# Performance work log

Hardware: AMD Instinct MI355X
Metric: run time of the kernel (lower is better)

## Reference

```python
import jax, jax.numpy as jnp
import numpy as np

N = 100000        # nodes
E = 1600000       # edges
NFEAT = 512
NLABEL = 64
NHID = 256
L_LAB = 5000


def _lin_init(key, fan_in, fan_out):
    kw, kb = jax.random.split(key)
    s = 1.0 / np.sqrt(fan_in).astype(np.float32)
    W = jax.random.uniform(kw, (fan_in, fan_out), jnp.float32, -s, s)
    b = jax.random.uniform(kb, (fan_out,), jnp.float32, -s, s)
    return W, b


def setup_inputs() -> dict:
    key = jax.random.key(0)
    ks = jax.random.split(key, 10)
    x = jax.random.normal(ks[0], (N, NFEAT), jnp.float32)
    y = jax.random.randint(ks[1], (N,), 0, NLABEL, jnp.int32)
    predictions = jax.random.uniform(ks[2], (N, NLABEL), dtype=jnp.float32)
    adj = jax.random.randint(ks[3], (2, E), 0, N, jnp.int32)
    idx_labeled = jax.random.randint(ks[4], (L_LAB,), 0, N, jnp.int32)
    d_in = NFEAT + NLABEL
    W0, b0 = _lin_init(ks[5], d_in, NHID)
    W1, b1 = _lin_init(ks[6], NHID, NHID)
    W2, b2 = _lin_init(ks[7], NHID, NHID)
    Wm0, bm0 = _lin_init(ks[8], NHID, 2 * NHID)
    Wm1, bm1 = _lin_init(ks[9], 2 * NHID, NLABEL)
    return dict(x=x, y=y, predictions=predictions, adj=adj, idx_labeled=idx_labeled,
                n_sample=1, W0=W0, b0=b0, W1=W1, b1=b1, W2=W2, b2=b2,
                Wm0=Wm0, bm0=bm0, Wm1=Wm1, bm1=bm1)


def reference(x, y, predictions, adj, idx_labeled, n_sample,
              W0, b0, W1, b1, W2, b2, Wm0, bm0, Wm1, bm1):
    n = x.shape[0]
    # --- pre_train label features: one_hot of (nlabel+2)-filled indices, labeled
    # nodes set to y; slicing to :nlabel makes out-of-range rows all-zero, which
    # jax.nn.one_hot does directly. -> [N, NLABEL]
    idx = jnp.full((n,), NLABEL + 2, jnp.int32).at[idx_labeled].set(y[idx_labeled])
    feats = jax.nn.one_hot(idx, NLABEL, dtype=x.dtype)
    h = jnp.concatenate([x, feats], axis=1)  # [N, nfeat+nlabel]

    # --- GCN normalization (improved=True: self-loop weight 2.0)
    loops = jnp.arange(n, dtype=adj.dtype)
    row = jnp.concatenate([adj[0], loops])  # message sources
    col = jnp.concatenate([adj[1], loops])  # aggregation targets
    ew = jnp.concatenate([jnp.ones((adj.shape[1],), jnp.float32),
                          jnp.full((n,), 2.0, jnp.float32)])
    deg = jax.ops.segment_sum(ew, col, num_segments=n)
    dinv = jnp.where(deg > 0, jax.lax.rsqrt(deg), 0.0)
    norm = dinv[row] * ew * dinv[col]  # [E+N]

    # --- 3 GCNConv layers: linear -> gather -> scale -> scatter-add -> +bias -> ReLU
    # (dropout p=0.5 treated as identity / eval mode)
    for W, b in ((W0, b0), (W1, b1), (W2, b2)):
        msg = (h @ W)[row] * norm[:, None]            # [E+N, NHID]
        h = jax.nn.relu(jax.ops.segment_sum(msg, col, num_segments=n) + b)

    # --- single-sample mean is identity; MLP head (num_linears=2) with ELU
    h = jax.nn.elu(h @ Wm0 + bm0)
    logits = h @ Wm1 + bm1
    return jax.nn.log_softmax(logits, axis=1)
```

## Files before the change

kernel.cpp:

```cpp
#include <hip/hip_runtime.h>
#include <math.h>

using f32x4  = __attribute__((ext_vector_type(4))) float;
using bf16x8 = __attribute__((ext_vector_type(8))) short;

constexpr int NFEAT = 512;
constexpr int NHID  = 256;
constexpr int NLAB  = 64;

__device__ __forceinline__ unsigned short f2bf(float f) {
    unsigned int u = __float_as_uint(f);
    u += 0x7FFFu + ((u >> 16) & 1u);
    return (unsigned short)(u >> 16);
}
__device__ __forceinline__ float bf2f(unsigned short s) {
    return __uint_as_float(((unsigned int)s) << 16);
}
__device__ __forceinline__ void gload_lds16(const void* g, void* l) {
    __builtin_amdgcn_global_load_lds(
        (const __attribute__((address_space(1))) unsigned int*)g,
        (__attribute__((address_space(3))) unsigned int*)l, 16, 0, 0);
}


__global__ void hist_kernel(const int* __restrict__ col, int* __restrict__ hist, int E) {
    int e = blockIdx.x * blockDim.x + threadIdx.x;
    if (e < E) atomicAdd(&hist[col[e]], 1);
}

__global__ void dinv_kernel(const int* __restrict__ hist, float* __restrict__ dinv, int n) {
    int i = blockIdx.x * blockDim.x + threadIdx.x;
    if (i < n) dinv[i] = rsqrtf((float)hist[i] + 2.0f);
}

__global__ void scan1_kernel(const int* __restrict__ hist, int* __restrict__ start,
                             int* __restrict__ bsum, int n) {
    __shared__ int sm[1024];
    const int t = threadIdx.x;
    const int i = blockIdx.x * 1024 + t;
    int v = (i < n) ? hist[i] : 0;
    sm[t] = v;
    __syncthreads();
    for (int off = 1; off < 1024; off <<= 1) {
        int x2 = (t >= off) ? sm[t - off] : 0;
        __syncthreads();
        sm[t] += x2;
        __syncthreads();
    }
    start[i] = sm[t] - v;
    if (t == 1023) bsum[blockIdx.x] = sm[1023];
}

__global__ void scan2_kernel(int* __restrict__ bsum, int nb) {
    __shared__ int sm[1024];
    const int t = threadIdx.x;
    int v = (t < nb) ? bsum[t] : 0;
    sm[t] = v;
    __syncthreads();
    for (int off = 1; off < 1024; off <<= 1) {
        int x2 = (t >= off) ? sm[t - off] : 0;
        __syncthreads();
        sm[t] += x2;
        __syncthreads();
    }
    if (t < nb) bsum[t] = sm[t] - v;
}

__global__ void scan3_kernel(int* __restrict__ start, int* __restrict__ cursor,
                             const int* __restrict__ bsum, int P) {
    int i = blockIdx.x * blockDim.x + threadIdx.x;
    if (i < P) {
        int v = start[i] + bsum[i >> 10];
        start[i] = v;
        if (i < P - 1) cursor[i] = v;
    }
}

__global__ void scatter_kernel(const int* __restrict__ row, const int* __restrict__ col,
                               const float* __restrict__ dinv, int* __restrict__ cursor,
                               int* __restrict__ ssrc, float* __restrict__ snorm, int E) {
    int e = blockIdx.x * blockDim.x + threadIdx.x;
    if (e < E) {
        int r = row[e], c = col[e];
        int p = atomicAdd(&cursor[c], 1);
        ssrc[p] = r;
        snorm[p] = dinv[r] * dinv[c];
    }
}

__global__ void labflag_kernel(const int* __restrict__ idxl, const int* __restrict__ y,
                               int* __restrict__ flag, int L) {
    int k = blockIdx.x * blockDim.x + threadIdx.x;
    if (k < L) {
        int node = idxl[k];
        flag[node] = y[node];
    }
}


__global__ void convT_kernel(const float* __restrict__ in, unsigned short* __restrict__ out,
                             int K, int Nc) {
    int idx = blockIdx.x * blockDim.x + threadIdx.x;
    if (idx < K * Nc) {
        int n = idx / K, k = idx - n * K;
        out[idx] = f2bf(in[(size_t)k * Nc + n]);
    }
}

__global__ void conv_kernel(const float* __restrict__ in, unsigned short* __restrict__ out, int total) {
    int idx = blockIdx.x * blockDim.x + threadIdx.x;
    if (idx < total) out[idx] = f2bf(in[idx]);
}


template<int EPI, bool AF32>
__global__ __launch_bounds__(256) void mfma_gemm(
    const unsigned short* __restrict__ A, const float* __restrict__ Af,
    const unsigned short* __restrict__ Bt, unsigned short* __restrict__ C,
    int M, int K, int N,
    const int* __restrict__ lflag, const unsigned short* __restrict__ Wlab,
    const float* __restrict__ bias) {
    __shared__ __align__(16) unsigned short lsA[128 * 64];
    __shared__ __align__(16) unsigned short lsB[128 * 64];
    const int t = threadIdx.x;
    const int wv = t >> 6, lane = t & 63;
    const int l16 = lane & 15, lk = lane >> 4;
    const int wr = wv >> 1, wc = wv & 1;
    const int row0 = blockIdx.x * 128, col0 = blockIdx.y * 128;

    f32x4 acc[4][4];
    const f32x4 fz = {0.f, 0.f, 0.f, 0.f};
    #pragma unroll
    for (int m = 0; m < 4; ++m)
        #pragma unroll
        for (int n = 0; n < 4; ++n) acc[m][n] = fz;

    for (int k0 = 0; k0 < K; k0 += 64) {
        #pragma unroll
        for (int q = 0; q < 4; ++q) {
            const int bc = wv * 256 + q * 64;
            const int c = bc + lane;
            const int row = c >> 3;
            const int kg = (c & 7) ^ (row & 7);
            const int arow = min(row0 + row, M - 1);
            if (AF32) {
                const float* src = Af + (size_t)arow * K + k0 + kg * 8;
                float4 f0 = *(const float4*)src;
                float4 f1 = *(const float4*)(src + 4);
                bf16x8 p;
                p[0] = (short)f2bf(f0.x); p[1] = (short)f2bf(f0.y);
                p[2] = (short)f2bf(f0.z); p[3] = (short)f2bf(f0.w);
                p[4] = (short)f2bf(f1.x); p[5] = (short)f2bf(f1.y);
                p[6] = (short)f2bf(f1.z); p[7] = (short)f2bf(f1.w);
                *(bf16x8*)&lsA[(size_t)c * 8] = p;
            } else {
                gload_lds16(A + (size_t)arow * K + k0 + kg * 8, &lsA[(size_t)bc * 8]);
            }
        }
        #pragma unroll
        for (int q = 0; q < 4; ++q) {
            const int bc = wv * 256 + q * 64;
            const int c = bc + lane;
            const int row = c >> 3;
            const int kg = (c & 7) ^ (row & 7);
            gload_lds16(Bt + (size_t)(col0 + row) * K + k0 + kg * 8, &lsB[(size_t)bc * 8]);
        }
        __syncthreads();
        #pragma unroll
        for (int kk = 0; kk < 2; ++kk) {
            bf16x8 a[4], b[4];
            #pragma unroll
            for (int m = 0; m < 4; ++m) {
                const int row = wr * 64 + m * 16 + l16;
                const int cc = row * 8 + ((kk * 4 + lk) ^ (row & 7));
                a[m] = *(const bf16x8*)&lsA[(size_t)cc * 8];
            }
            #pragma unroll
            for (int n = 0; n < 4; ++n) {
                const int row = wc * 64 + n * 16 + l16;
                const int cc = row * 8 + ((kk * 4 + lk) ^ (row & 7));
                b[n] = *(const bf16x8*)&lsB[(size_t)cc * 8];
            }
            #pragma unroll
            for (int m = 0; m < 4; ++m)
                #pragma unroll
                for (int n = 0; n < 4; ++n)
                    acc[m][n] = __builtin_amdgcn_mfma_f32_16x16x32_bf16(a[m], b[n], acc[m][n], 0, 0, 0);
        }
        __syncthreads();
    }

    #pragma unroll
    for (int m = 0; m < 4; ++m) {
        #pragma unroll
        for (int r = 0; r < 4; ++r) {
            const int grow = row0 + wr * 64 + m * 16 + lk * 4 + r;
            if (grow >= M) continue;
            int flag = -1;
            if (EPI == 1) flag = lflag[grow];
            #pragma unroll
            for (int n = 0; n < 4; ++n) {
                const int gcol = col0 + wc * 64 + n * 16 + l16;
                float v = acc[m][n][r];
                if (EPI == 1) { if (flag >= 0) v += bf2f(Wlab[flag * NHID + gcol]); }
                if (EPI == 2) { v += bias[gcol]; v = v > 0.f ? v : expm1f(v); }
                C[(size_t)grow * N + gcol] = f2bf(v);
            }
        }
    }
}


__global__ __launch_bounds__(256) void agg_bf16(
    const unsigned short* __restrict__ Z, const int* __restrict__ start,
    const int* __restrict__ ssrc, const float* __restrict__ snorm,
    const float* __restrict__ dinv, const float* __restrict__ bias,
    unsigned short* __restrict__ H, int M) {
    const int t = threadIdx.x;
    const int node = blockIdx.x * 4 + (t >> 6);
    if (node >= M) return;
    const int lane = t & 63;
    const int c0 = lane * 4;
    const float di = dinv[node];
    float a0, a1, a2, a3;
    {
        const float sw = 2.f * di * di;
        ushort4 z = *(const ushort4*)&Z[(size_t)node * NHID + c0];
        a0 = sw * bf2f(z.x); a1 = sw * bf2f(z.y);
        a2 = sw * bf2f(z.z); a3 = sw * bf2f(z.w);
    }
    const int s = start[node], e = start[node + 1];
    for (int base = s; base < e; base += 64) {
        const int cnt = min(64, e - base);
        int msrc = 0; float mnrm = 0.f;
        if (lane < cnt) { msrc = ssrc[base + lane]; mnrm = snorm[base + lane]; }
        for (int i = 0; i < cnt; ++i) {
            const int src = __shfl(msrc, i);
            const float nr = __shfl(mnrm, i);
            ushort4 zv = *(const ushort4*)&Z[(size_t)src * NHID + c0];
            a0 += nr * bf2f(zv.x); a1 += nr * bf2f(zv.y);
            a2 += nr * bf2f(zv.z); a3 += nr * bf2f(zv.w);
        }
    }
    float4 bb = *(const float4*)&bias[c0];
    ushort4 o;
    o.x = f2bf(fmaxf(a0 + bb.x, 0.f)); o.y = f2bf(fmaxf(a1 + bb.y, 0.f));
    o.z = f2bf(fmaxf(a2 + bb.z, 0.f)); o.w = f2bf(fmaxf(a3 + bb.w, 0.f));
    *(ushort4*)&H[(size_t)node * NHID + c0] = o;
}


__global__ __launch_bounds__(256) void logits_kernel(
    const unsigned short* __restrict__ A, const unsigned short* __restrict__ Bt,
    const float* __restrict__ bias, float* __restrict__ out, int M) {
    __shared__ __align__(16) unsigned short lsA[128 * 64];
    __shared__ __align__(16) unsigned short lsB[64 * 64];
    const int t = threadIdx.x;
    const int wv = t >> 6, lane = t & 63;
    const int l16 = lane & 15, lk = lane >> 4;
    const int row0 = blockIdx.x * 128;

    f32x4 acc[2][4];
    const f32x4 fz = {0.f, 0.f, 0.f, 0.f};
    #pragma unroll
    for (int m = 0; m < 2; ++m)
        #pragma unroll
        for (int n = 0; n < 4; ++n) acc[m][n] = fz;

    for (int k0 = 0; k0 < 512; k0 += 64) {
        #pragma unroll
        for (int q = 0; q < 4; ++q) {
            const int bc = wv * 256 + q * 64;
            const int c = bc + lane;
            const int row = c >> 3;
            const int kg = (c & 7) ^ (row & 7);
            gload_lds16(A + (size_t)min(row0 + row, M - 1) * 512 + k0 + kg * 8,
                        &lsA[(size_t)bc * 8]);
        }
        #pragma unroll
        for (int q = 0; q < 2; ++q) {
            const int bc = wv * 128 + q * 64;
            const int c = bc + lane;
            const int row = c >> 3;
            const int kg = (c & 7) ^ (row & 7);
            gload_lds16(Bt + (size_t)row * 512 + k0 + kg * 8, &lsB[(size_t)bc * 8]);
        }
        __syncthreads();
        #pragma unroll
        for (int kk = 0; kk < 2; ++kk) {
            bf16x8 a[2], b[4];
            #pragma unroll
            for (int m = 0; m < 2; ++m) {
                const int row = wv * 32 + m * 16 + l16;
                const int cc = row * 8 + ((kk * 4 + lk) ^ (row & 7));
                a[m] = *(const bf16x8*)&lsA[(size_t)cc * 8];
            }
            #pragma unroll
            for (int n = 0; n < 4; ++n) {
                const int row = n * 16 + l16;
                const int cc = row * 8 + ((kk * 4 + lk) ^ (row & 7));
                b[n] = *(const bf16x8*)&lsB[(size_t)cc * 8];
            }
            #pragma unroll
            for (int m = 0; m < 2; ++m)
                #pragma unroll
                for (int n = 0; n < 4; ++n)
                    acc[m][n] = __builtin_amdgcn_mfma_f32_16x16x32_bf16(a[m], b[n], acc[m][n], 0, 0, 0);
        }
        __syncthreads();
    }

    #pragma unroll
    for (int m = 0; m < 2; ++m) {
        #pragma unroll
        for (int r = 0; r < 4; ++r) {
            const int grow = row0 + wv * 32 + m * 16 + lk * 4 + r;
            float v[4];
            float mx = -3.4e38f;
            #pragma unroll
            for (int n = 0; n < 4; ++n) {
                v[n] = acc[m][n][r] + bias[n * 16 + l16];
                mx = fmaxf(mx, v[n]);
            }
            #pragma unroll
            for (int off = 1; off < 16; off <<= 1) mx = fmaxf(mx, __shfl_xor(mx, off));
            float s = 0.f;
            #pragma unroll
            for (int n = 0; n < 4; ++n) s += expf(v[n] - mx);
            #pragma unroll
            for (int off = 1; off < 16; off <<= 1) s += __shfl_xor(s, off);
            const float ls = logf(s);
            if (grow < M) {
                #pragma unroll
                for (int n = 0; n < 4; ++n)
                    out[(size_t)grow * NLAB + n * 16 + l16] = v[n] - mx - ls;
            }
        }
    }
}


extern "C" void kernel_launch(void* const* d_in, const int* in_sizes, int n_in,
                              void* d_out, int out_size, void* d_ws, size_t ws_size,
                              hipStream_t stream) {
    const float* x   = (const float*)d_in[0];
    const int*   y   = (const int*)  d_in[1];
    const int*   adj = (const int*)  d_in[3];
    const int*   idxl= (const int*)  d_in[4];
    const float* W0  = (const float*)d_in[6];
    const float* b0  = (const float*)d_in[7];
    const float* W1  = (const float*)d_in[8];
    const float* b1  = (const float*)d_in[9];
    const float* W2  = (const float*)d_in[10];
    const float* b2  = (const float*)d_in[11];
    const float* Wm0 = (const float*)d_in[12];
    const float* bm0 = (const float*)d_in[13];
    const float* Wm1 = (const float*)d_in[14];
    const float* bm1 = (const float*)d_in[15];

    const int N = in_sizes[0] / NFEAT;
    const int E = in_sizes[3] / 2;
    const int L = in_sizes[4];
    const int* erow = adj;
    const int* ecol = adj + E;

    char* ws = (char*)d_ws;
    size_t off = 0;
    auto alloc = [&](size_t bytes) -> void* {
        void* p = ws + off;
        off += (bytes + 255) & ~(size_t)255;
        return p;
    };
    const int P = N + 1;
    const int nb1 = (P + 1023) / 1024;
    unsigned short* Zb    = (unsigned short*)alloc((size_t)N * NHID * 2);
    unsigned short* Hb    = (unsigned short*)alloc((size_t)N * NHID * 2);
    int*   hist   = (int*)  alloc((size_t)N * 4);
    int*   startA = (int*)  alloc((size_t)nb1 * 1024 * 4);
    int*   cursor = (int*)  alloc((size_t)N * 4);
    float* dinv   = (float*)alloc((size_t)N * 4);
    int*   lflag  = (int*)  alloc((size_t)N * 4);
    int*   ssrc   = (int*)  alloc((size_t)E * 4);
    float* snorm  = (float*)alloc((size_t)E * 4);
    int*   bsum   = (int*)  alloc((size_t)1024 * 4);
    unsigned short* W0t   = (unsigned short*)alloc((size_t)256 * 512 * 2);
    unsigned short* W0lab = (unsigned short*)alloc((size_t)64 * 256 * 2);
    unsigned short* W1t   = (unsigned short*)alloc((size_t)256 * 256 * 2);
    unsigned short* W2t   = (unsigned short*)alloc((size_t)256 * 256 * 2);
    unsigned short* Wm0t  = (unsigned short*)alloc((size_t)512 * 256 * 2);
    unsigned short* Wm1t  = (unsigned short*)alloc((size_t)64 * 512 * 2);
    unsigned short* H1;
    {
        size_t need = (size_t)N * 512 * 2;
        if (off + need <= ws_size) H1 = (unsigned short*)alloc(need);
        else                       H1 = (unsigned short*)(void*)d_in[0];
    }

    hipMemsetAsync(hist, 0, (size_t)N * 4, stream);
    hipMemsetAsync(lflag, 0xFF, (size_t)N * 4, stream);

    const int TB = 256;
    hist_kernel<<<(E + TB - 1) / TB, TB, 0, stream>>>(ecol, hist, E);
    dinv_kernel<<<(N + TB - 1) / TB, TB, 0, stream>>>(hist, dinv, N);
    scan1_kernel<<<nb1, 1024, 0, stream>>>(hist, startA, bsum, N);
    scan2_kernel<<<1, 1024, 0, stream>>>(bsum, nb1);
    scan3_kernel<<<(P + TB - 1) / TB, TB, 0, stream>>>(startA, cursor, bsum, P);
    scatter_kernel<<<(E + TB - 1) / TB, TB, 0, stream>>>(erow, ecol, dinv, cursor, ssrc, snorm, E);
    labflag_kernel<<<(L + TB - 1) / TB, TB, 0, stream>>>(idxl, y, lflag, L);

    convT_kernel<<<(512 * 256 + TB - 1) / TB, TB, 0, stream>>>(W0, W0t, 512, 256);
    conv_kernel <<<(64 * 256 + TB - 1) / TB, TB, 0, stream>>>(W0 + (size_t)512 * 256, W0lab, 64 * 256);
    convT_kernel<<<(256 * 256 + TB - 1) / TB, TB, 0, stream>>>(W1, W1t, 256, 256);
    convT_kernel<<<(256 * 256 + TB - 1) / TB, TB, 0, stream>>>(W2, W2t, 256, 256);
    convT_kernel<<<(256 * 512 + TB - 1) / TB, TB, 0, stream>>>(Wm0, Wm0t, 256, 512);
    convT_kernel<<<(512 * 64 + TB - 1) / TB, TB, 0, stream>>>(Wm1, Wm1t, 512, 64);

    dim3 g2((N + 127) / 128, 2), g4((N + 127) / 128, 4);
    const int aggGrid = (N + 3) / 4;
    mfma_gemm<1, true ><<<g2, 256, 0, stream>>>(nullptr, x, W0t, Zb, N, 512, 256, lflag, W0lab, nullptr);
    agg_bf16<<<aggGrid, 256, 0, stream>>>(Zb, startA, ssrc, snorm, dinv, b0, Hb, N);
    mfma_gemm<0, false><<<g2, 256, 0, stream>>>(Hb, nullptr, W1t, Zb, N, 256, 256, nullptr, nullptr, nullptr);
    agg_bf16<<<aggGrid, 256, 0, stream>>>(Zb, startA, ssrc, snorm, dinv, b1, Hb, N);
    mfma_gemm<0, false><<<g2, 256, 0, stream>>>(Hb, nullptr, W2t, Zb, N, 256, 256, nullptr, nullptr, nullptr);
    agg_bf16<<<aggGrid, 256, 0, stream>>>(Zb, startA, ssrc, snorm, dinv, b2, Hb, N);
    mfma_gemm<2, false><<<g4, 256, 0, stream>>>(Hb, nullptr, Wm0t, H1, N, 256, 512, nullptr, nullptr, bm0);
    logits_kernel<<<(N + 127) / 128, 256, 0, stream>>>(H1, Wm1t, bm1, (float*)d_out, N);
}
```

Baseline: 1.166 ms.

## Fold source-side dinv into GEMM epilogue, drop per-edge norm, retile GEMM

The GEMM epilogue now scales each output row by dinv of that row. The per-edge norm array becomes unnecessary: aggregation sums pre-scaled source rows and multiplies once by the destination dinv, with the self-loop term 2*Zs[node]. This removes the snorm write in scatter and its reads in aggregation. The GEMM tile changes from 128x128 to 64x256, so one block covers all 256 output columns and A is loaded once. Aggregation is restructured so that two waves split the 256 columns of one node, each lane loads 8 bf16 values, four edges are processed in parallel per wave and the partial sums are combined with shuffle reductions. Rounding differs slightly because the dinv scaling is applied before the bf16 store.

```diff
diff --git a/kernel.cpp b/kernel.cpp
--- a/kernel.cpp
+++ b/kernel.cpp
@@ -3,6 +3,7 @@
 
 using f32x4  = __attribute__((ext_vector_type(4))) float;
 using bf16x8 = __attribute__((ext_vector_type(8))) short;
+using u16x8  = __attribute__((ext_vector_type(8))) unsigned short;
 
 constexpr int NFEAT = 512;
 constexpr int NHID  = 256;
@@ -77,14 +78,12 @@
 }
 
 __global__ void scatter_kernel(const int* __restrict__ row, const int* __restrict__ col,
-                               const float* __restrict__ dinv, int* __restrict__ cursor,
-                               int* __restrict__ ssrc, float* __restrict__ snorm, int E) {
+                               int* __restrict__ cursor, int* __restrict__ ssrc, int E) {
     int e = blockIdx.x * blockDim.x + threadIdx.x;
     if (e < E) {
         int r = row[e], c = col[e];
         int p = atomicAdd(&cursor[c], 1);
         ssrc[p] = r;
-        snorm[p] = dinv[r] * dinv[c];
     }
 }
 
@@ -119,14 +118,14 @@
     const unsigned short* __restrict__ Bt, unsigned short* __restrict__ C,
     int M, int K, int N,
     const int* __restrict__ lflag, const unsigned short* __restrict__ Wlab,
-    const float* __restrict__ bias) {
-    __shared__ __align__(16) unsigned short lsA[128 * 64];
-    __shared__ __align__(16) unsigned short lsB[128 * 64];
+    const float* __restrict__ bias, const float* __restrict__ dinv) {
+    __shared__ __align__(16) unsigned short lsA[64 * 64];
+    __shared__ __align__(16) unsigned short lsB[256 * 64];
     const int t = threadIdx.x;
     const int wv = t >> 6, lane = t & 63;
     const int l16 = lane & 15, lk = lane >> 4;
-    const int wr = wv >> 1, wc = wv & 1;
-    const int row0 = blockIdx.x * 128, col0 = blockIdx.y * 128;
+    const int row0 = blockIdx.x * 64;
+    const int col0 = blockIdx.y * 256;
 
     f32x4 acc[4][4];
     const f32x4 fz = {0.f, 0.f, 0.f, 0.f};
@@ -136,14 +135,13 @@
         for (int n = 0; n < 4; ++n) acc[m][n] = fz;
 
     for (int k0 = 0; k0 < K; k0 += 64) {
-        #pragma unroll
-        for (int q = 0; q < 4; ++q) {
-            const int bc = wv * 256 + q * 64;
-            const int c = bc + lane;
-            const int row = c >> 3;
-            const int kg = (c & 7) ^ (row & 7);
-            const int arow = min(row0 + row, M - 1);
-            if (AF32) {
+        if (AF32) {
+            #pragma unroll
+            for (int q = 0; q < 2; ++q) {
+                const int c = q * 256 + t;
+                const int row = c >> 3;
+                const int kg = (c & 7) ^ (row & 7);
+                const int arow = min(row0 + row, M - 1);
                 const float* src = Af + (size_t)arow * K + k0 + kg * 8;
                 float4 f0 = *(const float4*)src;
                 float4 f1 = *(const float4*)(src + 4);
@@ -153,13 +151,21 @@
                 p[4] = (short)f2bf(f1.x); p[5] = (short)f2bf(f1.y);
                 p[6] = (short)f2bf(f1.z); p[7] = (short)f2bf(f1.w);
                 *(bf16x8*)&lsA[(size_t)c * 8] = p;
-            } else {
+            }
+        } else {
+            #pragma unroll
+            for (int q = 0; q < 2; ++q) {
+                const int bc = q * 256 + wv * 64;
+                const int c = bc + lane;
+                const int row = c >> 3;
+                const int kg = (c & 7) ^ (row & 7);
+                const int arow = min(row0 + row, M - 1);
                 gload_lds16(A + (size_t)arow * K + k0 + kg * 8, &lsA[(size_t)bc * 8]);
             }
         }
         #pragma unroll
-        for (int q = 0; q < 4; ++q) {
-            const int bc = wv * 256 + q * 64;
+        for (int q = 0; q < 8; ++q) {
+            const int bc = q * 256 + wv * 64;
             const int c = bc + lane;
             const int row = c >> 3;
             const int kg = (c & 7) ^ (row & 7);
@@ -171,13 +177,13 @@
             bf16x8 a[4], b[4];
             #pragma unroll
             for (int m = 0; m < 4; ++m) {
-                const int row = wr * 64 + m * 16 + l16;
+                const int row = m * 16 + l16;
                 const int cc = row * 8 + ((kk * 4 + lk) ^ (row & 7));
                 a[m] = *(const bf16x8*)&lsA[(size_t)cc * 8];
             }
             #pragma unroll
             for (int n = 0; n < 4; ++n) {
-                const int row = wc * 64 + n * 16 + l16;
+                const int row = wv * 64 + n * 16 + l16;
                 const int cc = row * 8 + ((kk * 4 + lk) ^ (row & 7));
                 b[n] = *(const bf16x8*)&lsB[(size_t)cc * 8];
             }
@@ -194,15 +200,18 @@
     for (int m = 0; m < 4; ++m) {
         #pragma unroll
         for (int r = 0; r < 4; ++r) {
-            const int grow = row0 + wr * 64 + m * 16 + lk * 4 + r;
+            const int grow = row0 + m * 16 + lk * 4 + r;
             if (grow >= M) continue;
+            float dv = 1.0f;
+            if (EPI <= 1) dv = dinv[grow];
             int flag = -1;
             if (EPI == 1) flag = lflag[grow];
             #pragma unroll
             for (int n = 0; n < 4; ++n) {
-                const int gcol = col0 + wc * 64 + n * 16 + l16;
+                const int gcol = col0 + wv * 64 + n * 16 + l16;
                 float v = acc[m][n][r];
                 if (EPI == 1) { if (flag >= 0) v += bf2f(Wlab[flag * NHID + gcol]); }
+                if (EPI <= 1) { v *= dv; }
                 if (EPI == 2) { v += bias[gcol]; v = v > 0.f ? v : expm1f(v); }
                 C[(size_t)grow * N + gcol] = f2bf(v);
             }
@@ -212,41 +221,47 @@
 
 
 __global__ __launch_bounds__(256) void agg_bf16(
-    const unsigned short* __restrict__ Z, const int* __restrict__ start,
-    const int* __restrict__ ssrc, const float* __restrict__ snorm,
-    const float* __restrict__ dinv, const float* __restrict__ bias,
-    unsigned short* __restrict__ H, int M) {
+    const unsigned short* __restrict__ Zs, const int* __restrict__ start,
+    const int* __restrict__ ssrc, const float* __restrict__ dinv,
+    const float* __restrict__ bias, unsigned short* __restrict__ H, int M) {
     const int t = threadIdx.x;
-    const int node = blockIdx.x * 4 + (t >> 6);
+    const int wv = t >> 6, lane = t & 63;
+    const int node = blockIdx.x * 2 + (wv >> 1);
     if (node >= M) return;
-    const int lane = t & 63;
-    const int c0 = lane * 4;
-    const float di = dinv[node];
-    float a0, a1, a2, a3;
-    {
-        const float sw = 2.f * di * di;
-        ushort4 z = *(const ushort4*)&Z[(size_t)node * NHID + c0];
-        a0 = sw * bf2f(z.x); a1 = sw * bf2f(z.y);
-        a2 = sw * bf2f(z.z); a3 = sw * bf2f(z.w);
-    }
+    const int half = wv & 1;
+    const int g = lane >> 4, cl = lane & 15;
+    const int c0 = half * 128 + cl * 8;
+
+    float a[8] = {0.f, 0.f, 0.f, 0.f, 0.f, 0.f, 0.f, 0.f};
     const int s = start[node], e = start[node + 1];
-    for (int base = s; base < e; base += 64) {
-        const int cnt = min(64, e - base);
-        int msrc = 0; float mnrm = 0.f;
-        if (lane < cnt) { msrc = ssrc[base + lane]; mnrm = snorm[base + lane]; }
-        for (int i = 0; i < cnt; ++i) {
-            const int src = __shfl(msrc, i);
-            const float nr = __shfl(mnrm, i);
-            ushort4 zv = *(const ushort4*)&Z[(size_t)src * NHID + c0];
-            a0 += nr * bf2f(zv.x); a1 += nr * bf2f(zv.y);
-            a2 += nr * bf2f(zv.z); a3 += nr * bf2f(zv.w);
-        }
-    }
-    float4 bb = *(const float4*)&bias[c0];
-    ushort4 o;
-    o.x = f2bf(fmaxf(a0 + bb.x, 0.f)); o.y = f2bf(fmaxf(a1 + bb.y, 0.f));
-    o.z = f2bf(fmaxf(a2 + bb.z, 0.f)); o.w = f2bf(fmaxf(a3 + bb.w, 0.f));
-    *(ushort4*)&H[(size_t)node * NHID + c0] = o;
+    for (int base = s; base < e; base += 4) {
+        const int idx = base + g;
+        if (idx < e) {
+            const int src = ssrc[idx];
+            u16x8 z = *(const u16x8*)&Zs[(size_t)src * NHID + c0];
+            #pragma unroll
+            for (int j = 0; j < 8; ++j) a[j] += bf2f(z[j]);
+        }
+    }
+    #pragma unroll
+    for (int j = 0; j < 8; ++j) {
+        a[j] += __shfl_xor(a[j], 16);
+        a[j] += __shfl_xor(a[j], 32);
+    }
+    if (g == 0) {
+        u16x8 zs = *(const u16x8*)&Zs[(size_t)node * NHID + c0];
+        const float dv = dinv[node];
+        float4 bb0 = *(const float4*)&bias[c0];
+        float4 bb1 = *(const float4*)&bias[c0 + 4];
+        float bbf[8] = {bb0.x, bb0.y, bb0.z, bb0.w, bb1.x, bb1.y, bb1.z, bb1.w};
+        u16x8 o;
+        #pragma unroll
+        for (int j = 0; j < 8; ++j) {
+            float v = dv * (a[j] + 2.0f * bf2f(zs[j])) + bbf[j];
+            o[j] = f2bf(fmaxf(v, 0.f));
+        }
+        *(u16x8*)&H[(size_t)node * NHID + c0] = o;
+    }
 }
 
 
@@ -381,7 +396,6 @@
     float* dinv   = (float*)alloc((size_t)N * 4);
     int*   lflag  = (int*)  alloc((size_t)N * 4);
     int*   ssrc   = (int*)  alloc((size_t)E * 4);
-    float* snorm  = (float*)alloc((size_t)E * 4);
     int*   bsum   = (int*)  alloc((size_t)1024 * 4);
     unsigned short* W0t   = (unsigned short*)alloc((size_t)256 * 512 * 2);
     unsigned short* W0lab = (unsigned short*)alloc((size_t)64 * 256 * 2);
@@ -405,7 +419,7 @@
     scan1_kernel<<<nb1, 1024, 0, stream>>>(hist, startA, bsum, N);
     scan2_kernel<<<1, 1024, 0, stream>>>(bsum, nb1);
     scan3_kernel<<<(P + TB - 1) / TB, TB, 0, stream>>>(startA, cursor, bsum, P);
-    scatter_kernel<<<(E + TB - 1) / TB, TB, 0, stream>>>(erow, ecol, dinv, cursor, ssrc, snorm, E);
+    scatter_kernel<<<(E + TB - 1) / TB, TB, 0, stream>>>(erow, ecol, cursor, ssrc, E);
     labflag_kernel<<<(L + TB - 1) / TB, TB, 0, stream>>>(idxl, y, lflag, L);
 
     convT_kernel<<<(512 * 256 + TB - 1) / TB, TB, 0, stream>>>(W0, W0t, 512, 256);
@@ -415,14 +429,15 @@
     convT_kernel<<<(256 * 512 + TB - 1) / TB, TB, 0, stream>>>(Wm0, Wm0t, 256, 512);
     convT_kernel<<<(512 * 64 + TB - 1) / TB, TB, 0, stream>>>(Wm1, Wm1t, 512, 64);
 
-    dim3 g2((N + 127) / 128, 2), g4((N + 127) / 128, 4);
-    const int aggGrid = (N + 3) / 4;
-    mfma_gemm<1, true ><<<g2, 256, 0, stream>>>(nullptr, x, W0t, Zb, N, 512, 256, lflag, W0lab, nullptr);
-    agg_bf16<<<aggGrid, 256, 0, stream>>>(Zb, startA, ssrc, snorm, dinv, b0, Hb, N);
-    mfma_gemm<0, false><<<g2, 256, 0, stream>>>(Hb, nullptr, W1t, Zb, N, 256, 256, nullptr, nullptr, nullptr);
-    agg_bf16<<<aggGrid, 256, 0, stream>>>(Zb, startA, ssrc, snorm, dinv, b1, Hb, N);
-    mfma_gemm<0, false><<<g2, 256, 0, stream>>>(Hb, nullptr, W2t, Zb, N, 256, 256, nullptr, nullptr, nullptr);
-    agg_bf16<<<aggGrid, 256, 0, stream>>>(Zb, startA, ssrc, snorm, dinv, b2, Hb, N);
-    mfma_gemm<2, false><<<g4, 256, 0, stream>>>(Hb, nullptr, Wm0t, H1, N, 256, 512, nullptr, nullptr, bm0);
+    const int MB = (N + 63) / 64;
+    dim3 g1(MB, 1), gH(MB, 2);
+    const int aggGrid = (N + 1) / 2;
+    mfma_gemm<1, true ><<<g1, 256, 0, stream>>>(nullptr, x, W0t, Zb, N, 512, 256, lflag, W0lab, nullptr, dinv);
+    agg_bf16<<<aggGrid, 256, 0, stream>>>(Zb, startA, ssrc, dinv, b0, Hb, N);
+    mfma_gemm<0, false><<<g1, 256, 0, stream>>>(Hb, nullptr, W1t, Zb, N, 256, 256, nullptr, nullptr, nullptr, dinv);
+    agg_bf16<<<aggGrid, 256, 0, stream>>>(Zb, startA, ssrc, dinv, b1, Hb, N);
+    mfma_gemm<0, false><<<g1, 256, 0, stream>>>(Hb, nullptr, W2t, Zb, N, 256, 256, nullptr, nullptr, nullptr, dinv);
+    agg_bf16<<<aggGrid, 256, 0, stream>>>(Zb, startA, ssrc, dinv, b2, Hb, N);
+    mfma_gemm<2, false><<<gH, 256, 0, stream>>>(Hb, nullptr, Wm0t, H1, N, 256, 512, nullptr, nullptr, bm0, nullptr);
     logits_kernel<<<(N + 127) / 128, 256, 0, stream>>>(H1, Wm1t, bm1, (float*)d_out, N);
 }
```

Measured after the change: 1.195 ms. 2.5% more time.
